# Kernel tuning notes

Measured on AMD Instinct MI355X. Metric: run time of the kernel, lower is better.

## Reference

```python
import jax, jax.numpy as jnp
import numpy as np

B, T, D = 8, 1024, 256
H, KD = 8, 256          # keras MHA built with key_dim=embed_dim -> per-head dim = D
FF = 1024
WIN = 64                # causal sliding window size
G = 2                   # num_global_tokens (last-k tokens of the sequence)
EPS = 1e-6
NEG = -1e9


def _mha(q_in, kv_in, Wq, bq, Wk, bk, Wv, bv, Wo, bo, mask=None):
    """Keras-style MultiHeadAttention. q_in:[B,Tq,D], kv_in:[B,Ts,D] -> [B,Tq,D]."""
    q = jnp.einsum('btd,dhk->bthk', q_in, Wq) + bq
    k = jnp.einsum('bsd,dhk->bshk', kv_in, Wk) + bk
    v = jnp.einsum('bsd,dhk->bshk', kv_in, Wv) + bv
    s = jnp.einsum('bthk,bshk->bhts', q, k) / jnp.sqrt(jnp.asarray(KD, q.dtype))
    if mask is not None:
        s = jnp.where(mask, s, jnp.asarray(NEG, s.dtype))
    a = jax.nn.softmax(s, axis=-1)
    o = jnp.einsum('bhts,bshk->bthk', a, v)
    return jnp.einsum('bthk,hkd->btd', o, Wo) + bo


def _ln(x, g, b):
    m = jnp.mean(x, axis=-1, keepdims=True)
    v = jnp.mean(jnp.square(x - m), axis=-1, keepdims=True)
    return (x - m) * jax.lax.rsqrt(v + EPS) * g + b


def setup_inputs() -> dict:
    key = jax.random.key(0)
    ks = jax.random.split(key, 32)
    sp = 1.0 / np.sqrt(D)   # proj fan-in D
    so = 1.0 / np.sqrt(H * KD)

    def mha_params(k0):
        k = jax.random.split(k0, 4)
        return dict(
            Wq=jax.random.normal(k[0], (D, H, KD), jnp.float32) * sp,
            Wk=jax.random.normal(k[1], (D, H, KD), jnp.float32) * sp,
            Wv=jax.random.normal(k[2], (D, H, KD), jnp.float32) * sp,
            Wo=jax.random.normal(k[3], (H, KD, D), jnp.float32) * so,
        )
    lp = mha_params(ks[1])
    gp = mha_params(ks[2])
    inp = {
        'x': jax.random.normal(ks[0], (B, T, D), jnp.float32),
        'lWq': lp['Wq'], 'lbq': jnp.zeros((H, KD), jnp.float32),
        'lWk': lp['Wk'], 'lbk': jnp.zeros((H, KD), jnp.float32),
        'lWv': lp['Wv'], 'lbv': jnp.zeros((H, KD), jnp.float32),
        'lWo': lp['Wo'], 'lbo': jnp.zeros((D,), jnp.float32),
        'gWq': gp['Wq'], 'gbq': jnp.zeros((H, KD), jnp.float32),
        'gWk': gp['Wk'], 'gbk': jnp.zeros((H, KD), jnp.float32),
        'gWv': gp['Wv'], 'gbv': jnp.zeros((H, KD), jnp.float32),
        'gWo': gp['Wo'], 'gbo': jnp.zeros((D,), jnp.float32),
        'fW1': jax.random.normal(ks[3], (D, FF), jnp.float32) * sp,
        'fb1': jnp.zeros((FF,), jnp.float32),
        'fW2': jax.random.normal(ks[4], (FF, D), jnp.float32) * (1.0 / np.sqrt(FF)),
        'fb2': jnp.zeros((D,), jnp.float32),
        'ln1_g': jnp.ones((D,), jnp.float32), 'ln1_b': jnp.zeros((D,), jnp.float32),
        'ln2_g': jnp.ones((D,), jnp.float32), 'ln2_b': jnp.zeros((D,), jnp.float32),
    }
    return inp


def reference(x, lWq, lbq, lWk, lbk, lWv, lbv, lWo, lbo,
              gWq, gbq, gWk, gbk, gWv, gbv, gWo, gbo,
              fW1, fb1, fW2, fb2, ln1_g, ln1_b, ln2_g, ln2_b):
    i = jnp.arange(T)[:, None]
    j = jnp.arange(T)[None, :]
    win_mask = (j <= i) & (j > i - WIN)            # [T,T]
    win_mask = win_mask[None, None]                # [1,1,T,T]

    # Local window attention (the original per-timestep loop, fused via mask).
    local = _mha(x, x, lWq, lbq, lWk, lbk, lWv, lbv, lWo, lbo, mask=win_mask)

    # Global tokens: last G tokens attend to full sequence, then tokens attend to them.
    g = x[:, T - G:, :]                            # [B,G,D]
    g2 = _mha(g, x, gWq, gbq, gWk, gbk, gWv, gbv, gWo, gbo)
    gx = _mha(x, g2, gWq, gbq, gWk, gbk, gWv, gbv, gWo, gbo)

    attn_out = local + gx
    out1 = _ln(x + attn_out, ln1_g, ln1_b)
    ffn = jnp.maximum(out1 @ fW1 + fb1, 0.0) @ fW2 + fb2
    return _ln(out1 + ffn, ln2_g, ln2_b)
```

## Files before the change

### kernel.cpp

```cpp
#include <hip/hip_runtime.h>
#include <hip/hip_bf16.h>

#define B_ 8
#define T_ 1024
#define D_ 256
#define H_ 8
#define KD_ 256
#define HK_ 2048
#define FF_ 1024
#define WIN_ 64
#define BT_ 8192
#define S6_ 6144
#define S4_ 4096

using bf16 = __hip_bfloat16;
typedef float f32x4 __attribute__((ext_vector_type(4)));
typedef short s16x8 __attribute__((ext_vector_type(8)));

__device__ inline float b2f(bf16 h) { return __bfloat162float(h); }
__device__ inline float bs2f(short s) {
    unsigned int u = ((unsigned int)(unsigned short)s) << 16;
    return __builtin_bit_cast(float, u);
}
__device__ inline float us2f(unsigned short s) {
    unsigned int u = ((unsigned int)s) << 16;
    return __builtin_bit_cast(float, u);
}
__device__ inline unsigned short fbits(float x) { bf16 h = __float2bfloat16(x); return __builtin_bit_cast(unsigned short, h); }

__device__ __forceinline__ void stage16(const void* g, void* l) {
    __builtin_amdgcn_global_load_lds((const __attribute__((address_space(1))) void*)g,
                                     (__attribute__((address_space(3))) void*)l, 16, 0, 0);
}

__global__ __launch_bounds__(256) void f32_to_bf16_vec(const float* __restrict__ in, bf16* __restrict__ out, int n) {
    int i = (blockIdx.x * 256 + threadIdx.x) * 4;
    if (i + 3 < n) {
        float4 v = *(const float4*)(in + i);
        ushort4 o;
        o.x = fbits(v.x); o.y = fbits(v.y); o.z = fbits(v.z); o.w = fbits(v.w);
        *(ushort4*)(out + i) = o;
    }
}

struct TJob { const float* in; bf16* out; int R; int C; int os; int tile_start; };
struct TJobs { TJob j[10]; int total; };

__global__ void transpose_all(TJobs js) {
    __shared__ float tile[32][33];
    int bid = blockIdx.x;
    int ji = 0;
    while (ji < 9 && bid >= js.j[ji + 1].tile_start) ji++;
    TJob jb = js.j[ji];
    int t = bid - jb.tile_start;
    int tiles_x = jb.C / 32;
    int cb = (t % tiles_x) * 32, rb = (t / tiles_x) * 32;
    for (int k = 0; k < 4; k++) {
        int r = threadIdx.y + k * 8;
        tile[r][threadIdx.x] = jb.in[(size_t)(rb + r) * jb.C + cb + threadIdx.x];
    }
    __syncthreads();
    for (int k = 0; k < 4; k++) {
        int r = threadIdx.y + k * 8;
        jb.out[(size_t)(cb + r) * jb.os + rb + threadIdx.x] = __float2bfloat16(tile[threadIdx.x][r]);
    }
}

__global__ __launch_bounds__(256) void concat_bias(const float* a0, const float* a1, const float* a2,
                                                   const float* b0, const float* b1,
                                                   float* outL, float* outG) {
    int i = blockIdx.x * 256 + threadIdx.x;
    int seg = i >> 11, off = i & 2047;
    outL[i] = (seg == 0 ? a0 : seg == 1 ? a1 : a2)[off];
    if (i < 4096) outG[i] = (seg == 0 ? b0 : b1)[off];
}

template <int MODE, int BN>
__global__ __launch_bounds__(256) void gemm128(const bf16* __restrict__ A, const bf16* __restrict__ Bt,
                                               const float* __restrict__ bias, bf16* __restrict__ C,
                                               int M, int N, int K) {
    constexpr int NF = BN / 32;
    constexpr int ABUF = 128 * 64;
    constexpr int BBUF = BN * 64;
    constexpr int BUFE = ABUF + BBUF;
    constexpr int EC = BN + 8;
    constexpr int ARENA_E = (2 * BUFE > 128 * EC) ? 2 * BUFE : 128 * EC;
    __shared__ __align__(16) bf16 arena[ARENA_E];
    const int tid = threadIdx.x;
    const int w = tid >> 6, l = tid & 63;
    const int nwg = gridDim.x * gridDim.y;
    const int bid0 = blockIdx.y * gridDim.x + blockIdx.x;
    const int cpx = nwg >> 3;
    const int bid = (bid0 & 7) * cpx + (bid0 >> 3);
    const int m0 = (bid / gridDim.x) * 128, n0 = (bid % gridDim.x) * BN;
    const int wm = (w >> 1) * 64, wn = (w & 1) * (BN / 2);
    const int srow = w * 8 + (l >> 3);
    const int scol = (l & 7) * 8;
    const int ldsOff = w * 512;
    const int nt = K / 64;

    auto stageT = [&](int buf, int k0) {
        bf16* Ad = arena + buf * BUFE;
        bf16* Bd = Ad + ABUF;
#pragma unroll
        for (int j = 0; j < 4; j++)
            stage16(A + (size_t)(m0 + j * 32 + srow) * K + k0 + scol, &Ad[ldsOff + j * 2048]);
#pragma unroll
        for (int j = 0; j < NF; j++)
            stage16(Bt + (size_t)(n0 + j * 32 + srow) * K + k0 + scol, &Bd[ldsOff + j * 2048]);
    };

    f32x4 acc[4][NF] = {};
    stageT(0, 0);
    __syncthreads();
    int cur = 0;
    for (int t = 0; t < nt; t++) {
        if (t + 1 < nt) stageT(cur ^ 1, (t + 1) * 64);
        const bf16* As = arena + cur * BUFE;
        const bf16* Bs = As + ABUF;
#pragma unroll
        for (int ks = 0; ks < 2; ks++) {
            s16x8 a[4], b[NF];
#pragma unroll
            for (int mf = 0; mf < 4; mf++) a[mf] = *(const s16x8*)&As[(wm + mf * 16 + (l & 15)) * 64 + ks * 32 + (l >> 4) * 8];
#pragma unroll
            for (int nf = 0; nf < NF; nf++) b[nf] = *(const s16x8*)&Bs[(wn + nf * 16 + (l & 15)) * 64 + ks * 32 + (l >> 4) * 8];
            __builtin_amdgcn_s_setprio(1);
#pragma unroll
            for (int mf = 0; mf < 4; mf++)
#pragma unroll
                for (int nf = 0; nf < NF; nf++)
                    acc[mf][nf] = __builtin_amdgcn_mfma_f32_16x16x32_bf16(a[mf], b[nf], acc[mf][nf], 0, 0, 0);
            __builtin_amdgcn_s_setprio(0);
        }
        __syncthreads();
        cur ^= 1;
    }
    bf16* Es = arena;
#pragma unroll
    for (int mf = 0; mf < 4; mf++)
#pragma unroll
        for (int nf = 0; nf < NF; nf++)
#pragma unroll
            for (int r = 0; r < 4; r++) {
                int row = wm + mf * 16 + (l >> 4) * 4 + r;
                int col = wn + nf * 16 + (l & 15);
                float v = acc[mf][nf][r] + bias[n0 + col];
                if (MODE == 2) v = fmaxf(v, 0.f);
                Es[row * EC + col] = __float2bfloat16(v);
            }
    __syncthreads();
    constexpr int RPC = BN / 8;
    constexpr int CPT = (128 * BN) / (256 * 8);
#pragma unroll
    for (int c = 0; c < CPT; c++) {
        int lin = c * 256 + tid;
        int row = lin / RPC, cc = lin - row * RPC;
        s16x8 v = *(const s16x8*)&Es[row * EC + cc * 8];
        *(s16x8*)(C + (size_t)(m0 + row) * N + n0 + cc * 8) = v;
    }
}

__global__ __launch_bounds__(256) void local_attn(const bf16* __restrict__ QKV, bf16* __restrict__ O) {
    __shared__ bf16 U[256 * 72];
    __shared__ bf16 Ps[64][136];
    const int tid = threadIdx.x, l = tid & 63, w = tid >> 6;
    const int qt = blockIdx.x, bh = blockIdx.y;
    const int b = bh >> 3, h = bh & 7;
    const int qs = qt * 64;
    const int r0 = w * 16;
    const int lrow = tid >> 2, lc4 = (tid & 3) * 8;
    const size_t obase = (size_t)b * T_ * HK_ + h * KD_;

    s16x8 qa[8];
    {
        const bf16* qbase = QKV + (size_t)(b * T_ + qs + r0 + (l & 15)) * S6_ + h * KD_ + (l >> 4) * 8;
#pragma unroll
        for (int ks = 0; ks < 8; ks++) qa[ks] = *(const s16x8*)(qbase + ks * 32);
    }

    bf16(*Ks)[264] = (bf16(*)[264])U;
    {
        int tk = qs - 64 + lrow;
        const bf16* krow = QKV + (size_t)(b * T_ + tk) * S6_ + 2048 + h * KD_;
#pragma unroll
        for (int c = 0; c < 8; c++) {
            int col = lc4 + c * 32;
            uint4 val = {0, 0, 0, 0};
            if (tk >= 0) val = *(const uint4*)(krow + col);
            *(uint4*)&Ks[lrow][col] = val;
        }
    }
    __syncthreads();
    f32x4 sacc[8];
#pragma unroll
    for (int f = 0; f < 8; f++) sacc[f] = (f32x4){0.f, 0.f, 0.f, 0.f};
    __builtin_amdgcn_s_setprio(1);
#pragma unroll
    for (int nf = 0; nf < 4; nf++)
#pragma unroll
        for (int ks = 0; ks < 8; ks++) {
            s16x8 bb = *(const s16x8*)&Ks[nf * 16 + (l & 15)][ks * 32 + (l >> 4) * 8];
            sacc[nf] = __builtin_amdgcn_mfma_f32_16x16x32_bf16(qa[ks], bb, sacc[nf], 0, 0, 0);
        }
    __builtin_amdgcn_s_setprio(0);
    __syncthreads();
    {
        const bf16* krow = QKV + (size_t)(b * T_ + qs + lrow) * S6_ + 2048 + h * KD_;
#pragma unroll
        for (int c = 0; c < 8; c++) {
            int col = lc4 + c * 32;
            *(uint4*)&Ks[lrow][col] = *(const uint4*)(krow + col);
        }
    }
    __syncthreads();
    __builtin_amdgcn_s_setprio(1);
#pragma unroll
    for (int nf = 0; nf < 4; nf++)
#pragma unroll
        for (int ks = 0; ks < 8; ks++) {
            s16x8 bb = *(const s16x8*)&Ks[nf * 16 + (l & 15)][ks * 32 + (l >> 4) * 8];
            sacc[4 + nf] = __builtin_amdgcn_mfma_f32_16x16x32_bf16(qa[ks], bb, sacc[4 + nf], 0, 0, 0);
        }
    __builtin_amdgcn_s_setprio(0);

    uint4 vreg[8];
    {
        int tk = qs - 64 + lrow;
        const bf16* vrow = QKV + (size_t)(b * T_ + tk) * S6_ + 4096 + h * KD_;
#pragma unroll
        for (int c = 0; c < 8; c++) {
            uint4 v = {0, 0, 0, 0};
            if (tk >= 0) v = *(const uint4*)(vrow + lc4 + c * 32);
            vreg[c] = v;
        }
    }

#pragma unroll
    for (int r = 0; r < 4; r++) {
        int i = qs + r0 + (l >> 4) * 4 + r;
#pragma unroll
        for (int f = 0; f < 8; f++) {
            int j = qs - 64 + f * 16 + (l & 15);
            bool valid = (j >= 0) && (j <= i) && (j > i - WIN_);
            sacc[f][r] = valid ? sacc[f][r] * (1.f / 16.f) : -1e9f;
        }
        float mm = -1e30f;
#pragma unroll
        for (int f = 0; f < 8; f++) mm = fmaxf(mm, sacc[f][r]);
        mm = fmaxf(mm, __shfl_xor(mm, 1, 64));
        mm = fmaxf(mm, __shfl_xor(mm, 2, 64));
        mm = fmaxf(mm, __shfl_xor(mm, 4, 64));
        mm = fmaxf(mm, __shfl_xor(mm, 8, 64));
        float ss = 0.f;
#pragma unroll
        for (int f = 0; f < 8; f++) {
            float e = __expf(sacc[f][r] - mm);
            sacc[f][r] = e;
            ss += e;
        }
        ss += __shfl_xor(ss, 1, 64);
        ss += __shfl_xor(ss, 2, 64);
        ss += __shfl_xor(ss, 4, 64);
        ss += __shfl_xor(ss, 8, 64);
        float inv = 1.f / ss;
#pragma unroll
        for (int f = 0; f < 8; f++) sacc[f][r] *= inv;
    }
    __syncthreads();

    bf16(*VT)[72] = (bf16(*)[72])U;
#pragma unroll
    for (int f = 0; f < 8; f++)
#pragma unroll
        for (int r = 0; r < 4; r++)
            Ps[r0 + (l >> 4) * 4 + r][f * 16 + (l & 15)] = __float2bfloat16(sacc[f][r]);
#pragma unroll
    for (int c = 0; c < 8; c++) {
        int col = lc4 + c * 32;
        bf16 tmp[8];
        *(uint4*)tmp = vreg[c];
        for (int e = 0; e < 8; e++) VT[col + e][lrow] = tmp[e];
    }
    __syncthreads();
    {
        const bf16* vrow = QKV + (size_t)(b * T_ + qs + lrow) * S6_ + 4096 + h * KD_;
#pragma unroll
        for (int c = 0; c < 8; c++) vreg[c] = *(const uint4*)(vrow + lc4 + c * 32);
    }

    f32x4 oacc[16];
#pragma unroll
    for (int nf = 0; nf < 16; nf++) oacc[nf] = (f32x4){0.f, 0.f, 0.f, 0.f};
    for (int kb = 0; kb < 2; kb++) {
#pragma unroll
        for (int ks = 0; ks < 2; ks++) {
            s16x8 a = *(const s16x8*)&Ps[r0 + (l & 15)][kb * 64 + ks * 32 + (l >> 4) * 8];
            __builtin_amdgcn_s_setprio(1);
#pragma unroll
            for (int nf = 0; nf < 16; nf++) {
                s16x8 bb = *(const s16x8*)&VT[nf * 16 + (l & 15)][ks * 32 + (l >> 4) * 8];
                oacc[nf] = __builtin_amdgcn_mfma_f32_16x16x32_bf16(a, bb, oacc[nf], 0, 0, 0);
            }
            __builtin_amdgcn_s_setprio(0);
        }
        if (kb == 0) {
            __syncthreads();
#pragma unroll
            for (int c = 0; c < 8; c++) {
                int col = lc4 + c * 32;
                bf16 tmp[8];
                *(uint4*)tmp = vreg[c];
                for (int e = 0; e < 8; e++) VT[col + e][lrow] = tmp[e];
            }
            __syncthreads();
        }
    }
#pragma unroll
    for (int nf = 0; nf < 16; nf++)
#pragma unroll
        for (int r = 0; r < 4; r++) {
            int row = r0 + (l >> 4) * 4 + r;
            int col = nf * 16 + (l & 15);
            O[obase + (size_t)(qs + row) * HK_ + col] = __float2bfloat16(oacc[nf][r]);
        }
}

__global__ __launch_bounds__(256) void qg_kernel(const float* __restrict__ x, const bf16* __restrict__ gwq_t,
                                                 const float* __restrict__ gbq, float* __restrict__ qg) {
    __shared__ float xs[256];
    int bi = blockIdx.x, ch = blockIdx.y, tid = threadIdx.x;
    int b = bi >> 1, i = bi & 1;
    xs[tid] = x[((size_t)b * T_ + (T_ - 2 + i)) * D_ + tid];
    __syncthreads();
    int hk = ch * 256 + tid;
    const bf16* wr = gwq_t + (size_t)hk * D_;
    float acc = gbq[hk];
    for (int c = 0; c < 32; c++) {
        s16x8 wv = *(const s16x8*)&wr[c * 8];
#pragma unroll
        for (int e = 0; e < 8; e++) acc += xs[c * 8 + e] * bs2f(wv[e]);
    }
    qg[(size_t)bi * HK_ + hk] = acc;
}

__global__ __launch_bounds__(256) void g2_scores(const float* __restrict__ qg, const bf16* __restrict__ KVg,
                                                 float* __restrict__ sc) {
    __shared__ float qf[2][256];
    int bh = blockIdx.x, ch = blockIdx.y;
    int b = bh >> 3, h = bh & 7;
    int tid = threadIdx.x;
    for (int i = 0; i < 2; i++)
        qf[i][tid] = qg[(size_t)(b * 2 + i) * HK_ + h * KD_ + tid];
    __syncthreads();
    int t = ch * 256 + tid;
    const bf16* kr = &KVg[((size_t)(b * T_ + t)) * S4_ + h * KD_];
    float a0 = 0.f, a1 = 0.f;
    for (int c = 0; c < 32; c++) {
        s16x8 kv = *(const s16x8*)&kr[c * 8];
#pragma unroll
        for (int e = 0; e < 8; e++) {
            float kf = bs2f(kv[e]);
            a0 += kf * qf[0][c * 8 + e];
            a1 += kf * qf[1][c * 8 + e];
        }
    }
    sc[((size_t)bh * 2 + 0) * T_ + t] = a0 * (1.f / 16.f);
    sc[((size_t)bh * 2 + 1) * T_ + t] = a1 * (1.f / 16.f);
}

__global__ __launch_bounds__(256) void g2_softmax(float* __restrict__ sc) {
    __shared__ float red[4];
    int bh = blockIdx.x, tid = threadIdx.x;
    int w = tid >> 6;
    for (int i = 0; i < 2; i++) {
        float* row = &sc[((size_t)bh * 2 + i) * T_];
        float vals[4];
        float m = -1e30f;
        for (int c = 0; c < 4; c++) {
            vals[c] = row[tid + 256 * c];
            m = fmaxf(m, vals[c]);
        }
        for (int s = 32; s >= 1; s >>= 1) m = fmaxf(m, __shfl_xor(m, s, 64));
        if ((tid & 63) == 0) red[w] = m;
        __syncthreads();
        m = fmaxf(fmaxf(red[0], red[1]), fmaxf(red[2], red[3]));
        __syncthreads();
        float s = 0.f;
        for (int c = 0; c < 4; c++) {
            vals[c] = __expf(vals[c] - m);
            s += vals[c];
        }
        for (int d = 32; d >= 1; d >>= 1) s += __shfl_xor(s, d, 64);
        if ((tid & 63) == 0) red[w] = s;
        __syncthreads();
        s = red[0] + red[1] + red[2] + red[3];
        float inv = 1.f / s;
        for (int c = 0; c < 4; c++) row[tid + 256 * c] = vals[c] * inv;
        __syncthreads();
    }
}

__global__ __launch_bounds__(256) void g2_pv(const float* __restrict__ sc, const bf16* __restrict__ KVg,
                                             float* __restrict__ og_part) {
    __shared__ float p2[2][256];
    int bh = blockIdx.x, ch = blockIdx.y;
    int b = bh >> 3, h = bh & 7;
    int tid = threadIdx.x;
    for (int i = 0; i < 2; i++) p2[i][tid] = sc[((size_t)bh * 2 + i) * T_ + ch * 256 + tid];
    __syncthreads();
    const bf16* vb = &KVg[((size_t)(b * T_ + ch * 256)) * S4_ + 2048 + h * KD_ + tid];
    float a0 = 0.f, a1 = 0.f;
    for (int t = 0; t < 256; t++) {
        float vv = b2f(vb[(size_t)t * S4_]);
        a0 += p2[0][t] * vv;
        a1 += p2[1][t] * vv;
    }
    og_part[((size_t)(bh * 4 + ch) * 2 + 0) * KD_ + tid] = a0;
    og_part[((size_t)(bh * 4 + ch) * 2 + 1) * KD_ + tid] = a1;
}

__global__ __launch_bounds__(256) void g2_red(const float* __restrict__ og_part, float* __restrict__ og2) {
    int idx = blockIdx.x * 256 + threadIdx.x;
    int kd = idx & 255, i = (idx >> 8) & 1, h = (idx >> 9) & 7, b = idx >> 12;
    int bh = b * 8 + h;
    float s = 0.f;
    for (int ch = 0; ch < 4; ch++) s += og_part[((size_t)(bh * 4 + ch) * 2 + i) * KD_ + kd];
    og2[(size_t)(b * 2 + i) * 2048 + h * 256 + kd] = s;
}

__global__ __launch_bounds__(256) void g2_lin(const float* __restrict__ og2, const bf16* __restrict__ gwoT,
                                              const float* __restrict__ gbo, float* __restrict__ g2buf) {
    int bi = blockIdx.x, tid = threadIdx.x;
    int d = blockIdx.y * 16 + (tid >> 4);
    int s16i = tid & 15;
    const float* ogr = og2 + (size_t)bi * 2048 + s16i * 128;
    const bf16* wr = gwoT + (size_t)d * HK_ + s16i * 128;
    float acc = 0.f;
    for (int c = 0; c < 16; c++) {
        s16x8 wv = *(const s16x8*)&wr[c * 8];
#pragma unroll
        for (int e = 0; e < 8; e++) acc += ogr[c * 8 + e] * bs2f(wv[e]);
    }
    acc += __shfl_xor(acc, 1, 64);
    acc += __shfl_xor(acc, 2, 64);
    acc += __shfl_xor(acc, 4, 64);
    acc += __shfl_xor(acc, 8, 64);
    if (s16i == 0) g2buf[(size_t)bi * 256 + d] = acc + gbo[d];
}

__global__ __launch_bounds__(256) void g2_kv(const float* __restrict__ g2buf, const bf16* __restrict__ gwk_t,
                                             const float* __restrict__ gbk, const bf16* __restrict__ gwv_t,
                                             const float* __restrict__ gbv, bf16* __restrict__ K2,
                                             bf16* __restrict__ V2) {
    __shared__ float g2s[256];
    int bi = blockIdx.x, ch = blockIdx.y;
    int tid = threadIdx.x;
    g2s[tid] = g2buf[(size_t)bi * 256 + tid];
    __syncthreads();
    int hk = ch * 256 + tid;
    const bf16* rk = &gwk_t[(size_t)hk * D_];
    const bf16* rv = &gwv_t[(size_t)hk * D_];
    float ak = gbk[hk], av = gbv[hk];
    for (int c = 0; c < 32; c++) {
        s16x8 kw = *(const s16x8*)&rk[c * 8];
        s16x8 vw = *(const s16x8*)&rv[c * 8];
#pragma unroll
        for (int e = 0; e < 8; e++) {
            float g = g2s[c * 8 + e];
            ak += g * bs2f(kw[e]);
            av += g * bs2f(vw[e]);
        }
    }
    K2[(size_t)bi * HK_ + hk] = __float2bfloat16(ak);
    V2[(size_t)bi * HK_ + hk] = __float2bfloat16(av);
}

__global__ __launch_bounds__(256) void a2w2_kernel(const bf16* __restrict__ K2, const bf16* __restrict__ V2,
                                                   const bf16* __restrict__ gwq_t, const bf16* __restrict__ gwoT,
                                                   const float* __restrict__ gbq, float* __restrict__ A2,
                                                   float* __restrict__ W2, float* __restrict__ c2) {
    __shared__ float k2s[256], v2s[256];
    __shared__ float red[4];
    int bi = blockIdx.x, h = blockIdx.y, tid = threadIdx.x;
    k2s[tid] = b2f(K2[(size_t)bi * HK_ + h * 256 + tid]);
    v2s[tid] = b2f(V2[(size_t)bi * HK_ + h * 256 + tid]);
    __syncthreads();
    float accA = 0.f;
    const bf16* wq = gwq_t + (size_t)(h * 256) * D_ + tid;
    for (int kd = 0; kd < 256; kd++)
        accA += k2s[kd] * b2f(wq[(size_t)kd * D_]);
    float accW = 0.f;
    const bf16* wo = gwoT + (size_t)tid * HK_ + h * 256;
    for (int c = 0; c < 32; c++) {
        s16x8 wv = *(const s16x8*)&wo[c * 8];
#pragma unroll
        for (int e = 0; e < 8; e++) accW += v2s[c * 8 + e] * bs2f(wv[e]);
    }
    int o = (bi * 8 + h) * 256 + tid;
    A2[o] = accA;
    W2[o] = accW;
    float pc = gbq[h * 256 + tid] * k2s[tid];
#pragma unroll
    for (int m = 32; m >= 1; m >>= 1) pc += __shfl_xor(pc, m, 64);
    if ((tid & 63) == 0) red[tid >> 6] = pc;
    __syncthreads();
    if (tid == 0) c2[bi * 8 + h] = red[0] + red[1] + red[2] + red[3];
}

__global__ __launch_bounds__(256) void gx_fused(const float* __restrict__ x, const float* __restrict__ A2,
                                                const float* __restrict__ W2, const float* __restrict__ c2,
                                                const float* __restrict__ gbo, bf16* __restrict__ attnG) {
    int w = threadIdx.x >> 6, l = threadIdx.x & 63;
    int t = blockIdx.x * 4 + w;
    int b = t >> 10;
    float4 x4 = *(const float4*)(x + (size_t)t * D_ + l * 4);
    float p[8][2];
#pragma unroll
    for (int h = 0; h < 8; h++)
#pragma unroll
        for (int i = 0; i < 2; i++) {
            const float* a = A2 + ((size_t)((b * 2 + i) * 8 + h)) * 256 + l * 4;
            float4 a4 = *(const float4*)a;
            float dt = x4.x * a4.x + x4.y * a4.y + x4.z * a4.z + x4.w * a4.w;
#pragma unroll
            for (int m = 32; m >= 1; m >>= 1) dt += __shfl_xor(dt, m, 64);
            p[h][i] = dt;
        }
    float4 gb = *(const float4*)(gbo + l * 4);
    float o0 = gb.x, o1 = gb.y, o2 = gb.z, o3 = gb.w;
#pragma unroll
    for (int h = 0; h < 8; h++) {
        float s0 = (p[h][0] + c2[(b * 2 + 0) * 8 + h]) * (1.f / 16.f);
        float s1 = (p[h][1] + c2[(b * 2 + 1) * 8 + h]) * (1.f / 16.f);
        float mx = fmaxf(s0, s1);
        float e0 = __expf(s0 - mx), e1 = __expf(s1 - mx);
        float inv = 1.f / (e0 + e1);
        float p0 = e0 * inv, p1 = e1 * inv;
        float4 w0 = *(const float4*)(W2 + ((size_t)((b * 2 + 0) * 8 + h)) * 256 + l * 4);
        float4 w1 = *(const float4*)(W2 + ((size_t)((b * 2 + 1) * 8 + h)) * 256 + l * 4);
        o0 += p0 * w0.x + p1 * w1.x;
        o1 += p0 * w0.y + p1 * w1.y;
        o2 += p0 * w0.z + p1 * w1.z;
        o3 += p0 * w0.w + p1 * w1.w;
    }
    ushort4 ou;
    ou.x = fbits(o0); ou.y = fbits(o1); ou.z = fbits(o2); ou.w = fbits(o3);
    *(ushort4*)(attnG + (size_t)t * D_ + l * 4) = ou;
}

__global__ __launch_bounds__(256) void ln_kernel(const float* __restrict__ a, const bf16* __restrict__ b2,
                                                 const bf16* __restrict__ c, const float* __restrict__ g,
                                                 const float* __restrict__ bia, float* __restrict__ outf,
                                                 bf16* __restrict__ outb) {
    int w = threadIdx.x >> 6, l = threadIdx.x & 63;
    int row = blockIdx.x * 4 + w;
    size_t base = (size_t)row * D_ + l * 4;
    float4 av = *(const float4*)(a + base);
    ushort4 bv = *(const ushort4*)(b2 + base);
    float vv[4];
    vv[0] = av.x + us2f(bv.x); vv[1] = av.y + us2f(bv.y);
    vv[2] = av.z + us2f(bv.z); vv[3] = av.w + us2f(bv.w);
    if (c) {
        ushort4 cv = *(const ushort4*)(c + base);
        vv[0] += us2f(cv.x); vv[1] += us2f(cv.y); vv[2] += us2f(cv.z); vv[3] += us2f(cv.w);
    }
    float s = vv[0] + vv[1] + vv[2] + vv[3];
#pragma unroll
    for (int m = 32; m >= 1; m >>= 1) s += __shfl_xor(s, m, 64);
    float mean = s * (1.f / 256.f);
    float q = 0.f;
#pragma unroll
    for (int e = 0; e < 4; e++) {
        float d = vv[e] - mean;
        q += d * d;
    }
#pragma unroll
    for (int m = 32; m >= 1; m >>= 1) q += __shfl_xor(q, m, 64);
    float rs = rsqrtf(q * (1.f / 256.f) + 1e-6f);
    float4 gv = *(const float4*)(g + l * 4);
    float4 biv = *(const float4*)(bia + l * 4);
    float o0 = (vv[0] - mean) * rs * gv.x + biv.x;
    float o1 = (vv[1] - mean) * rs * gv.y + biv.y;
    float o2 = (vv[2] - mean) * rs * gv.z + biv.z;
    float o3 = (vv[3] - mean) * rs * gv.w + biv.w;
    if (outf) *(float4*)(outf + base) = (float4){o0, o1, o2, o3};
    if (outb) {
        ushort4 ou;
        ou.x = fbits(o0); ou.y = fbits(o1); ou.z = fbits(o2); ou.w = fbits(o3);
        *(ushort4*)(outb + base) = ou;
    }
}

extern "C" void kernel_launch(void* const* d_in, const int* in_sizes, int n_in, void* d_out, int out_size,
                              void* d_ws, size_t ws_size, hipStream_t stream) {
    const float* x = (const float*)d_in[0];
    const float* lWq = (const float*)d_in[1];  const float* lbq = (const float*)d_in[2];
    const float* lWk = (const float*)d_in[3];  const float* lbk = (const float*)d_in[4];
    const float* lWv = (const float*)d_in[5];  const float* lbv = (const float*)d_in[6];
    const float* lWo = (const float*)d_in[7];  const float* lbo = (const float*)d_in[8];
    const float* gWq = (const float*)d_in[9];  const float* gbq = (const float*)d_in[10];
    const float* gWk = (const float*)d_in[11]; const float* gbk = (const float*)d_in[12];
    const float* gWv = (const float*)d_in[13]; const float* gbv = (const float*)d_in[14];
    const float* gWo = (const float*)d_in[15]; const float* gbo = (const float*)d_in[16];
    const float* fW1 = (const float*)d_in[17]; const float* fb1 = (const float*)d_in[18];
    const float* fW2 = (const float*)d_in[19]; const float* fb2 = (const float*)d_in[20];
    const float* ln1g = (const float*)d_in[21]; const float* ln1b = (const float*)d_in[22];
    const float* ln2g = (const float*)d_in[23]; const float* ln2b = (const float*)d_in[24];

    char* ws = (char*)d_ws;
    size_t off = 0;
    auto alloc = [&](size_t bytes) -> char* {
        char* p = ws + off;
        off = (off + bytes + 255) & ~(size_t)255;
        return p;
    };
    bf16* xb = (bf16*)alloc((size_t)BT_ * D_ * 2);
    bf16* WcatL = (bf16*)alloc((size_t)S6_ * D_ * 2);
    bf16* WcatG = (bf16*)alloc((size_t)S4_ * D_ * 2);
    bf16* gwq_t = (bf16*)alloc((size_t)HK_ * D_ * 2);
    bf16* woL = (bf16*)alloc((size_t)D_ * HK_ * 2);
    bf16* gwoT = (bf16*)alloc((size_t)D_ * HK_ * 2);
    bf16* fw1_t = (bf16*)alloc((size_t)FF_ * D_ * 2);
    bf16* fw2_t = (bf16*)alloc((size_t)D_ * FF_ * 2);
    float* bcatL = (float*)alloc((size_t)S6_ * 4);
    float* bcatG = (float*)alloc((size_t)S4_ * 4);
    bf16* QKV = (bf16*)alloc((size_t)BT_ * S6_ * 2);
    bf16* Ob = (bf16*)alloc((size_t)BT_ * HK_ * 2);
    bf16* attnL = (bf16*)alloc((size_t)BT_ * D_ * 2);
    bf16* attnG = (bf16*)alloc((size_t)BT_ * D_ * 2);
    float* out1 = (float*)alloc((size_t)BT_ * D_ * 4);
    float* sc = (float*)alloc((size_t)B_ * H_ * 2 * T_ * 4);
    float* og_part = (float*)alloc((size_t)B_ * H_ * 4 * 2 * KD_ * 4);
    float* og2 = (float*)alloc((size_t)B_ * 2 * HK_ * 4);
    float* g2buf = (float*)alloc((size_t)B_ * 2 * D_ * 4);
    float* qg = (float*)alloc((size_t)B_ * 2 * HK_ * 4);
    bf16* K2 = (bf16*)alloc((size_t)B_ * 2 * HK_ * 2);
    bf16* V2 = (bf16*)alloc((size_t)B_ * 2 * HK_ * 2);
    float* A2 = (float*)alloc((size_t)16 * 8 * 256 * 4);
    float* W2 = (float*)alloc((size_t)16 * 8 * 256 * 4);
    float* c2 = (float*)alloc((size_t)16 * 8 * 4);
    bf16* KVg = QKV;
    bf16* hid = QKV;
    bf16* ffn = (bf16*)((char*)QKV + (32u << 20));
    bf16* out1b = (bf16*)((char*)QKV + (48u << 20));

    f32_to_bf16_vec<<<(BT_ * D_) / 1024, 256, 0, stream>>>(x, xb, BT_ * D_);
    {
        TJobs js;
        int t = 0;
        auto add = [&](int i, const float* in, bf16* out, int R, int C, int os) {
            js.j[i] = {in, out, R, C, os, t};
            t += (R / 32) * (C / 32);
        };
        add(0, lWq, WcatL, D_, HK_, D_);
        add(1, lWk, WcatL + (size_t)2048 * D_, D_, HK_, D_);
        add(2, lWv, WcatL + (size_t)4096 * D_, D_, HK_, D_);
        add(3, gWk, WcatG, D_, HK_, D_);
        add(4, gWv, WcatG + (size_t)2048 * D_, D_, HK_, D_);
        add(5, gWq, gwq_t, D_, HK_, D_);
        add(6, lWo, woL, HK_, D_, HK_);
        add(7, gWo, gwoT, HK_, D_, HK_);
        add(8, fW1, fw1_t, D_, FF_, D_);
        add(9, fW2, fw2_t, FF_, D_, FF_);
        js.total = t;
        transpose_all<<<t, dim3(32, 8), 0, stream>>>(js);
    }
    concat_bias<<<S6_ / 256, 256, 0, stream>>>(lbq, lbk, lbv, gbk, gbv, bcatL, bcatG);
    qg_kernel<<<dim3(16, 8), 256, 0, stream>>>(x, gwq_t, gbq, qg);

    gemm128<1, 128><<<dim3(S6_ / 128, BT_ / 128), 256, 0, stream>>>(xb, WcatL, bcatL, QKV, BT_, S6_, D_);
    local_attn<<<dim3(T_ / 64, B_ * H_), 256, 0, stream>>>(QKV, Ob);
    gemm128<1, 64><<<dim3(D_ / 64, BT_ / 128), 256, 0, stream>>>(Ob, woL, lbo, attnL, BT_, D_, HK_);

    gemm128<1, 128><<<dim3(S4_ / 128, BT_ / 128), 256, 0, stream>>>(xb, WcatG, bcatG, KVg, BT_, S4_, D_);
    g2_scores<<<dim3(B_ * H_, T_ / 256), 256, 0, stream>>>(qg, KVg, sc);
    g2_softmax<<<B_ * H_, 256, 0, stream>>>(sc);
    g2_pv<<<dim3(B_ * H_, 4), 256, 0, stream>>>(sc, KVg, og_part);
    g2_red<<<128, 256, 0, stream>>>(og_part, og2);
    g2_lin<<<dim3(B_ * 2, 16), 256, 0, stream>>>(og2, gwoT, gbo, g2buf);
    g2_kv<<<dim3(B_ * 2, HK_ / 256), 256, 0, stream>>>(g2buf, WcatG, gbk, WcatG + (size_t)2048 * D_, gbv, K2, V2);
    a2w2_kernel<<<dim3(16, 8), 256, 0, stream>>>(K2, V2, gwq_t, gwoT, gbq, A2, W2, c2);
    gx_fused<<<BT_ / 4, 256, 0, stream>>>(x, A2, W2, c2, gbo, attnG);

    ln_kernel<<<BT_ / 4, 256, 0, stream>>>(x, attnL, attnG, ln1g, ln1b, out1, out1b);
    gemm128<2, 128><<<dim3(FF_ / 128, BT_ / 128), 256, 0, stream>>>(out1b, fw1_t, fb1, hid, BT_, FF_, D_);
    gemm128<1, 64><<<dim3(D_ / 64, BT_ / 128), 256, 0, stream>>>(hid, fw2_t, fb2, ffn, BT_, D_, FF_);
    ln_kernel<<<BT_ / 4, 256, 0, stream>>>(out1, ffn, nullptr, ln2g, ln2b, (float*)d_out, nullptr);
}
```

Before: 280.7 us.

## Swizzle GEMM LDS tiles, drop XCD block remap, keep LN residual in bf16

The GEMM kernel now XOR-swizzles the 16-byte column chunk by row when staging A/B tiles into LDS. It un-swizzles the same way on the MFMA fragment reads, which is meant to remove LDS bank conflicts on the 128-byte tile rows. The XCD-aware block-id remapping is removed in favour of plain blockIdx tiling, which may change L2 locality across chiplets. The layer-norm kernel is templated so that the first LN no longer writes an fp32 out1 copy, and the second LN reads the bf16 out1b as its residual. This saves memory traffic but rounds the residual to bf16.

```diff
diff --git a/kernel.cpp b/kernel.cpp
--- a/kernel.cpp
+++ b/kernel.cpp
@@ -88,14 +88,10 @@
     __shared__ __align__(16) bf16 arena[ARENA_E];
     const int tid = threadIdx.x;
     const int w = tid >> 6, l = tid & 63;
-    const int nwg = gridDim.x * gridDim.y;
-    const int bid0 = blockIdx.y * gridDim.x + blockIdx.x;
-    const int cpx = nwg >> 3;
-    const int bid = (bid0 & 7) * cpx + (bid0 >> 3);
-    const int m0 = (bid / gridDim.x) * 128, n0 = (bid % gridDim.x) * BN;
+    const int m0 = blockIdx.y * 128, n0 = blockIdx.x * BN;
     const int wm = (w >> 1) * 64, wn = (w & 1) * (BN / 2);
     const int srow = w * 8 + (l >> 3);
-    const int scol = (l & 7) * 8;
+    const int scol = ((l & 7) ^ (l >> 3)) * 8;
     const int ldsOff = w * 512;
     const int nt = K / 64;
 
@@ -122,9 +118,17 @@
         for (int ks = 0; ks < 2; ks++) {
             s16x8 a[4], b[NF];
 #pragma unroll
-            for (int mf = 0; mf < 4; mf++) a[mf] = *(const s16x8*)&As[(wm + mf * 16 + (l & 15)) * 64 + ks * 32 + (l >> 4) * 8];
-#pragma unroll
-            for (int nf = 0; nf < NF; nf++) b[nf] = *(const s16x8*)&Bs[(wn + nf * 16 + (l & 15)) * 64 + ks * 32 + (l >> 4) * 8];
+            for (int mf = 0; mf < 4; mf++) {
+                int ar = wm + mf * 16 + (l & 15);
+                int ch = (ks * 4 + (l >> 4)) ^ (ar & 7);
+                a[mf] = *(const s16x8*)&As[ar * 64 + ch * 8];
+            }
+#pragma unroll
+            for (int nf = 0; nf < NF; nf++) {
+                int br = wn + nf * 16 + (l & 15);
+                int ch = (ks * 4 + (l >> 4)) ^ (br & 7);
+                b[nf] = *(const s16x8*)&Bs[br * 64 + ch * 8];
+            }
             __builtin_amdgcn_s_setprio(1);
 #pragma unroll
             for (int mf = 0; mf < 4; mf++)
@@ -549,20 +553,26 @@
     *(ushort4*)(attnG + (size_t)t * D_ + l * 4) = ou;
 }
 
-__global__ __launch_bounds__(256) void ln_kernel(const float* __restrict__ a, const bf16* __restrict__ b2,
+template <typename TA, bool HASC>
+__global__ __launch_bounds__(256) void ln_kernel(const TA* __restrict__ a, const bf16* __restrict__ b2,
                                                  const bf16* __restrict__ c, const float* __restrict__ g,
                                                  const float* __restrict__ bia, float* __restrict__ outf,
                                                  bf16* __restrict__ outb) {
     int w = threadIdx.x >> 6, l = threadIdx.x & 63;
     int row = blockIdx.x * 4 + w;
     size_t base = (size_t)row * D_ + l * 4;
-    float4 av = *(const float4*)(a + base);
-    ushort4 bv = *(const ushort4*)(b2 + base);
     float vv[4];
-    vv[0] = av.x + us2f(bv.x); vv[1] = av.y + us2f(bv.y);
-    vv[2] = av.z + us2f(bv.z); vv[3] = av.w + us2f(bv.w);
-    if (c) {
-        ushort4 cv = *(const ushort4*)(c + base);
+    if constexpr (sizeof(TA) == 4) {
+        float4 av = *(const float4*)((const float*)a + base);
+        vv[0] = av.x; vv[1] = av.y; vv[2] = av.z; vv[3] = av.w;
+    } else {
+        ushort4 av = *(const ushort4*)((const unsigned short*)a + base);
+        vv[0] = us2f(av.x); vv[1] = us2f(av.y); vv[2] = us2f(av.z); vv[3] = us2f(av.w);
+    }
+    ushort4 bv = *(const ushort4*)((const unsigned short*)b2 + base);
+    vv[0] += us2f(bv.x); vv[1] += us2f(bv.y); vv[2] += us2f(bv.z); vv[3] += us2f(bv.w);
+    if constexpr (HASC) {
+        ushort4 cv = *(const ushort4*)((const unsigned short*)c + base);
         vv[0] += us2f(cv.x); vv[1] += us2f(cv.y); vv[2] += us2f(cv.z); vv[3] += us2f(cv.w);
     }
     float s = vv[0] + vv[1] + vv[2] + vv[3];
@@ -629,7 +639,6 @@
     bf16* Ob = (bf16*)alloc((size_t)BT_ * HK_ * 2);
     bf16* attnL = (bf16*)alloc((size_t)BT_ * D_ * 2);
     bf16* attnG = (bf16*)alloc((size_t)BT_ * D_ * 2);
-    float* out1 = (float*)alloc((size_t)BT_ * D_ * 4);
     float* sc = (float*)alloc((size_t)B_ * H_ * 2 * T_ * 4);
     float* og_part = (float*)alloc((size_t)B_ * H_ * 4 * 2 * KD_ * 4);
     float* og2 = (float*)alloc((size_t)B_ * 2 * HK_ * 4);
@@ -683,8 +692,8 @@
     a2w2_kernel<<<dim3(16, 8), 256, 0, stream>>>(K2, V2, gwq_t, gwoT, gbq, A2, W2, c2);
     gx_fused<<<BT_ / 4, 256, 0, stream>>>(x, A2, W2, c2, gbo, attnG);
 
-    ln_kernel<<<BT_ / 4, 256, 0, stream>>>(x, attnL, attnG, ln1g, ln1b, out1, out1b);
+    ln_kernel<float, true><<<BT_ / 4, 256, 0, stream>>>(x, attnL, attnG, ln1g, ln1b, nullptr, out1b);
     gemm128<2, 128><<<dim3(FF_ / 128, BT_ / 128), 256, 0, stream>>>(out1b, fw1_t, fb1, hid, BT_, FF_, D_);
     gemm128<1, 64><<<dim3(D_ / 64, BT_ / 128), 256, 0, stream>>>(hid, fw2_t, fb2, ffn, BT_, D_, FF_);
-    ln_kernel<<<BT_ / 4, 256, 0, stream>>>(out1, ffn, nullptr, ln2g, ln2b, (float*)d_out, nullptr);
-}
+    ln_kernel<bf16, false><<<BT_ / 4, 256, 0, stream>>>(out1b, ffn, nullptr, ln2g, ln2b, (float*)d_out, nullptr);
+}
```

Result: faster. 271.6 us (-3.3%).
